# Kernel tuning notes

Measured on AMD Instinct MI355X. Metric: run time of the kernel, lower is better.

The kernel has to match this reference:

```python
import jax, jax.numpy as jnp
import numpy as np

N_NODES_PER_SLICE = 1024  # n_physical_qubits + 1


def _gcn_layer(x, row, col, n_nodes, W, b):
    """PyG GCNConv: add self-loops, symmetric deg normalization, linear, scatter-add, +bias."""
    sl = jnp.arange(n_nodes, dtype=row.dtype)
    row_f = jnp.concatenate([row, sl])
    col_f = jnp.concatenate([col, sl])
    deg = jax.ops.segment_sum(jnp.ones_like(col_f, dtype=x.dtype), col_f, num_segments=n_nodes)
    dinv = jnp.where(deg > 0, jax.lax.rsqrt(deg), 0.0)
    norm = dinv[row_f] * dinv[col_f]            # [E_total]
    h = x @ W                                    # [n_nodes, out]
    msg = h[row_f] * norm[:, None]               # gather + scale
    out = jax.ops.segment_sum(msg, col_f, num_segments=n_nodes)  # scatter-add
    return out + b


def reference(edge_index, qubit_embeddings, W1, b1, W2, b2, W3, b3):
    B = edge_index.shape[0]
    npn = N_NODES_PER_SLICE
    n_nodes = B * npn
    # Batch.from_data_list: offset each slice's edge_index by b * npn, tile node features
    offsets = (jnp.arange(B, dtype=edge_index.dtype) * npn)[:, None]  # [B,1]
    row = (edge_index[:, 0, :] + offsets).reshape(-1)  # [B*E]
    col = (edge_index[:, 1, :] + offsets).reshape(-1)
    x = jnp.tile(qubit_embeddings, (B, 1))             # [B*npn, d0]
    for W, b in ((W1, b1), (W2, b2), (W3, b3)):
        x = jax.nn.relu(_gcn_layer(x, row, col, n_nodes, W, b))
    return x


def setup_inputs() -> dict:
    key = jax.random.key(0)
    ks = jax.random.split(key, 8)
    B, E, d = 512, 2048, 128
    return {
        "edge_index": jax.random.randint(ks[0], (B, 2, E), 0, N_NODES_PER_SLICE, dtype=jnp.int64 if jax.config.jax_enable_x64 else jnp.int32),
        "qubit_embeddings": jax.random.normal(ks[1], (N_NODES_PER_SLICE, d), dtype=jnp.float32),
        "W1": jax.random.normal(ks[2], (d, d), dtype=jnp.float32) * (1.0 / np.sqrt(d)),
        "b1": jnp.zeros((d,), dtype=jnp.float32),
        "W2": jax.random.normal(ks[3], (d, d), dtype=jnp.float32) * (1.0 / np.sqrt(d)),
        "b2": jnp.zeros((d,), dtype=jnp.float32),
        "W3": jax.random.normal(ks[4], (d, d), dtype=jnp.float32) * (1.0 / np.sqrt(d)),
        "b3": jnp.zeros((d,), dtype=jnp.float32),
    }
```

## Files before the change

kernel.cpp:

```cpp
#include <hip/hip_runtime.h>

#define NPN   1024
#define NB    512
#define NE_S  2048
#define DD    128
#define NN    (NB * NPN)
#define NE    (NB * NE_S)

typedef short s16x8 __attribute__((ext_vector_type(8)));
typedef float f32x4 __attribute__((ext_vector_type(4)));

static __device__ __forceinline__ unsigned short f2bf(float f) {
    unsigned u = __builtin_bit_cast(unsigned, f);
    unsigned r = (u + 0x7FFFu + ((u >> 16) & 1u)) >> 16;
    return (unsigned short)r;
}
static __device__ __forceinline__ float bf2f(unsigned short h) {
    unsigned u = ((unsigned)h) << 16;
    return __builtin_bit_cast(float, u);
}


__global__ void k_count(const int* __restrict__ ei, int* __restrict__ deg) {
    int t = blockIdx.x * 256 + threadIdx.x;
    int b = t >> 11, e = t & (NE_S - 1);
    int col = ei[b * (2 * NE_S) + NE_S + e];
    atomicAdd(&deg[b * NPN + col], 1);
}

__global__ void k_dinv(const int* __restrict__ deg, float* __restrict__ dinv) {
    int i = blockIdx.x * 256 + threadIdx.x;
    dinv[i] = rsqrtf((float)(deg[i] + 1));
}

__global__ __launch_bounds__(1024) void k_scan(const int* __restrict__ deg,
                                               int* __restrict__ coff,
                                               int* __restrict__ cur) {
    __shared__ int s[NPN];
    int b = blockIdx.x, t = threadIdx.x;
    int v = deg[b * NPN + t];
    s[t] = v;
    __syncthreads();
    for (int off = 1; off < NPN; off <<= 1) {
        int add = (t >= off) ? s[t - off] : 0;
        __syncthreads();
        s[t] += add;
        __syncthreads();
    }
    coff[b * NPN + t] = b * NE_S + (s[t] - v);
    cur[b * NPN + t] = 0;
}

__global__ void k_fill(const int* __restrict__ ei, const float* __restrict__ dinv,
                       const int* __restrict__ coff, int* __restrict__ cur,
                       int2* __restrict__ cmeta) {
    int t = blockIdx.x * 256 + threadIdx.x;
    int b = t >> 11, e = t & (NE_S - 1);
    int r = ei[b * (2 * NE_S) + e];
    int c = ei[b * (2 * NE_S) + NE_S + e];
    int gr = b * NPN + r, gc = b * NPN + c;
    int pos = coff[gc] + atomicAdd(&cur[gc], 1);
    float nw = dinv[gr] * dinv[gc];
    cmeta[pos] = make_int2(r | (c << 16), __builtin_bit_cast(int, nw));
}


__global__ __launch_bounds__(256) void k_wsplit(const float* __restrict__ W,
                                                short* __restrict__ WTh,
                                                short* __restrict__ WTl) {
    int idx = blockIdx.x * 256 + threadIdx.x;
    int k = idx >> 7, n = idx & 127;
    float f = W[idx];
    unsigned short h = f2bf(f);
    unsigned short l = f2bf(f - bf2f(h));
    WTh[n * DD + k] = (short)h;
    WTl[n * DD + k] = (short)l;
}


__global__ __launch_bounds__(512, 8) void k_layer(const float* __restrict__ x,
                                                  unsigned gmask,
                                                  const short* __restrict__ WTh,
                                                  const short* __restrict__ WTl,
                                                  const float* __restrict__ bias,
                                                  const float* __restrict__ dinv,
                                                  const int* __restrict__ coff,
                                                  const int2* __restrict__ cmeta,
                                                  float* __restrict__ out) {
    __shared__ float sBuf[64 * DD];
    float* sAcc = sBuf;
    char*  sH   = (char*)sBuf;
    char*  sL   = (char*)sBuf + 16384;

    int t = threadIdx.x;
    int wave = t >> 6, lane = t & 63;
    int wb = (int)((blockIdx.x & 7) * 1024 + (blockIdx.x >> 3));
    int m0 = wb * 64;
    int sbase = (wb >> 4) << 10;

    int n  = lane & 15;
    int kq = lane >> 4;

    int r0g = m0 + wave * 8;
    int wlo = (m0 - sbase) + wave * 8;
    int eBeg = __builtin_amdgcn_readfirstlane(coff[r0g]);
    int eEnd = __builtin_amdgcn_readfirstlane((r0g + 8 < NN) ? coff[r0g + 8] : NE);

    int c0 = eBeg;
    int nC0 = eEnd - c0; nC0 = nC0 > 64 ? 64 : nC0;
    int2 md = make_int2((int)0xFFFF0000u, 0);
    if (lane < nC0) md = cmeta[c0 + lane];

    {
        float2 sv[8]; float dvv[8];
        #pragma unroll
        for (int i = 0; i < 8; ++i) {
            int g = m0 + wave * 8 + i;
            dvv[i] = dinv[g];
            sv[i] = *(const float2*)&x[(size_t)((unsigned)g & gmask) * DD + lane * 2];
        }
        #pragma unroll
        for (int i = 0; i < 8; ++i) {
            int row = wave * 8 + i;
            float s = dvv[i] * dvv[i];
            sAcc[row * DD + lane]      = s * sv[i].x;
            sAcc[row * DD + 64 + lane] = s * sv[i].y;
        }
    }

    float ax = 0.f, ay = 0.f;
    int curRow = -1;
    int nC = nC0;
    while (true) {
        int nB = (nC + 15) & ~15;
        for (int b0 = 0; b0 < nB; b0 += 16) {
            float2 v[16];
            #pragma unroll
            for (int j = 0; j < 16; ++j) {
                int sj = __builtin_amdgcn_readlane(md.x, b0 + j) & 0xFFFF;
                v[j] = *(const float2*)&x[(size_t)((unsigned)(sbase + sj) & gmask) * DD + lane * 2];
            }
            #pragma unroll
            for (int j = 0; j < 16; ++j) {
                int pj = __builtin_amdgcn_readlane(md.x, b0 + j);
                int dst = (int)(((unsigned)pj) >> 16);
                float w = __builtin_bit_cast(float, __builtin_amdgcn_readlane(md.y, b0 + j));
                if (dst != curRow) {
                    unsigned rl = (unsigned)(curRow - wlo);
                    if (rl < 8u) {
                        int row = wave * 8 + (int)rl;
                        atomicAdd(&sAcc[row * DD + lane],      ax);
                        atomicAdd(&sAcc[row * DD + 64 + lane], ay);
                    }
                    curRow = dst; ax = 0.f; ay = 0.f;
                }
                ax = fmaf(w, v[j].x, ax);
                ay = fmaf(w, v[j].y, ay);
            }
        }
        c0 += 64;
        if (c0 >= eEnd) break;
        nC = eEnd - c0; nC = nC > 64 ? 64 : nC;
        md = make_int2((int)0xFFFF0000u, 0);
        if (lane < nC) md = cmeta[c0 + lane];
    }
    {
        unsigned rl = (unsigned)(curRow - wlo);
        if (rl < 8u) {
            int row = wave * 8 + (int)rl;
            atomicAdd(&sAcc[row * DD + lane],      ax);
            atomicAdd(&sAcc[row * DD + 64 + lane], ay);
        }
    }
    __syncthreads();

    float fe[8], fo[8];
    #pragma unroll
    for (int i = 0; i < 8; ++i) {
        int row = wave * 8 + i;
        fe[i] = sAcc[row * DD + lane];
        fo[i] = sAcc[row * DD + 64 + lane];
    }
    __syncthreads();
    #pragma unroll
    for (int i = 0; i < 8; ++i) {
        int row = wave * 8 + i;
        unsigned short hx = f2bf(fe[i]); unsigned short lx = f2bf(fe[i] - bf2f(hx));
        unsigned short hy = f2bf(fo[i]); unsigned short ly = f2bf(fo[i] - bf2f(hy));
        unsigned bo = ((unsigned)row * 256u + (unsigned)lane * 4u) ^ ((unsigned)(row & 7) << 4);
        *(unsigned*)(sH + bo) = ((unsigned)hy << 16) | hx;
        *(unsigned*)(sL + bo) = ((unsigned)ly << 16) | lx;
    }
    __syncthreads();

    f32x4 acc[4];
    #pragma unroll
    for (int m = 0; m < 4; ++m) acc[m] = (f32x4){0.f, 0.f, 0.f, 0.f};

    const short* bhp = &WTh[(wave * 16 + n) * DD + kq * 8];
    const short* blp = &WTl[(wave * 16 + n) * DD + kq * 8];
    #pragma unroll
    for (int ks = 0; ks < 4; ++ks) {
        s16x8 bhv = *(const s16x8*)(bhp + ks * 32);
        s16x8 blv = *(const s16x8*)(blp + ks * 32);
        #pragma unroll
        for (int m = 0; m < 4; ++m) {
            int row = m * 16 + n;
            unsigned bo = ((unsigned)row * 256u + (unsigned)(ks * 64 + kq * 16))
                          ^ ((unsigned)(row & 7) << 4);
            s16x8 ah = *(const s16x8*)(sH + bo);
            s16x8 al = *(const s16x8*)(sL + bo);
            acc[m] = __builtin_amdgcn_mfma_f32_16x16x32_bf16(ah, bhv, acc[m], 0, 0, 0);
            acc[m] = __builtin_amdgcn_mfma_f32_16x16x32_bf16(ah, blv, acc[m], 0, 0, 0);
            acc[m] = __builtin_amdgcn_mfma_f32_16x16x32_bf16(al, bhv, acc[m], 0, 0, 0);
        }
    }

    int col = wave * 16 + n;
    float bv = bias[col];
    #pragma unroll
    for (int m = 0; m < 4; ++m) {
        #pragma unroll
        for (int r = 0; r < 4; ++r) {
            int row = m * 16 + kq * 4 + r;
            float vv = acc[m][r] + bv;
            out[(size_t)(m0 + row) * DD + col] = fmaxf(vv, 0.f);
        }
    }
}


extern "C" void kernel_launch(void* const* d_in, const int* in_sizes, int n_in,
                              void* d_out, int out_size, void* d_ws, size_t ws_size,
                              hipStream_t stream) {
    const int*   ei  = (const int*)d_in[0];
    const float* emb = (const float*)d_in[1];
    const float* W1  = (const float*)d_in[2];
    const float* b1  = (const float*)d_in[3];
    const float* W2  = (const float*)d_in[4];
    const float* b2  = (const float*)d_in[5];
    const float* W3  = (const float*)d_in[6];
    const float* b3  = (const float*)d_in[7];
    float* out = (float*)d_out;

    float* x_mid = (float*)d_ws;
    float* dinv  = x_mid + (size_t)NN * DD;
    int*   deg   = (int*)(dinv + NN);
    int*   coff  = deg + NN;
    int*   cur   = coff + NN;
    int2*  cmeta = (int2*)(cur + NN);
    short* WTh1  = (short*)(cmeta + NE);
    short* WTl1  = WTh1 + DD * DD;
    short* WTh2  = WTl1 + DD * DD;
    short* WTl2  = WTh2 + DD * DD;
    short* WTh3  = WTl2 + DD * DD;
    short* WTl3  = WTh3 + DD * DD;

    hipMemsetAsync(deg, 0, NN * sizeof(int), stream);
    k_count<<<NE / 256, 256, 0, stream>>>(ei, deg);
    k_dinv<<<NN / 256, 256, 0, stream>>>(deg, dinv);
    k_scan<<<NB, NPN, 0, stream>>>(deg, coff, cur);
    k_fill<<<NE / 256, 256, 0, stream>>>(ei, dinv, coff, cur, cmeta);

    k_wsplit<<<64, 256, 0, stream>>>(W1, WTh1, WTl1);
    k_wsplit<<<64, 256, 0, stream>>>(W2, WTh2, WTl2);
    k_wsplit<<<64, 256, 0, stream>>>(W3, WTh3, WTl3);

    k_layer<<<NN / 64, 512, 0, stream>>>(emb, NPN - 1, WTh1, WTl1, b1,
                                         dinv, coff, cmeta, out);
    k_layer<<<NN / 64, 512, 0, stream>>>(out, 0xFFFFFFFFu, WTh2, WTl2, b2,
                                         dinv, coff, cmeta, x_mid);
    k_layer<<<NN / 64, 512, 0, stream>>>(x_mid, 0xFFFFFFFFu, WTh3, WTl3, b3,
                                         dinv, coff, cmeta, out);
}
```

Before: 1.123 ms.

## Split wave halves across two edges with float4 gathers and per-edge LDS atomics

Each wave now handles two edges per step, one per 32-lane half, and each lane gathers a float4 from the source row instead of a float2. The per-lane running accumulator keyed on destination row is dropped, and every edge's weighted message goes straight into LDS with four atomic adds. The aim is wider, more coalesced global gathers and half as many serial gather iterations. The cost is many more LDS atomics, since every edge now issues them rather than only at destination changes, and the two halves can contend on the same row. The self-loop initialisation and the later readback are also switched to vector loads and stores.

```diff
diff --git a/kernel.cpp b/kernel.cpp
--- a/kernel.cpp
+++ b/kernel.cpp
@@ -94,6 +94,7 @@
 
     int t = threadIdx.x;
     int wave = t >> 6, lane = t & 63;
+    int half = lane >> 5, li = lane & 31;
     int wb = (int)((blockIdx.x & 7) * 1024 + (blockIdx.x >> 3));
     int m0 = wb * 64;
     int sbase = (wb >> 4) << 10;
@@ -111,51 +112,44 @@
     int2 md = make_int2((int)0xFFFF0000u, 0);
     if (lane < nC0) md = cmeta[c0 + lane];
 
-    {
-        float2 sv[8]; float dvv[8];
-        #pragma unroll
-        for (int i = 0; i < 8; ++i) {
-            int g = m0 + wave * 8 + i;
-            dvv[i] = dinv[g];
-            sv[i] = *(const float2*)&x[(size_t)((unsigned)g & gmask) * DD + lane * 2];
-        }
-        #pragma unroll
-        for (int i = 0; i < 8; ++i) {
-            int row = wave * 8 + i;
-            float s = dvv[i] * dvv[i];
-            sAcc[row * DD + lane]      = s * sv[i].x;
-            sAcc[row * DD + 64 + lane] = s * sv[i].y;
-        }
-    }
-
-    float ax = 0.f, ay = 0.f;
-    int curRow = -1;
+    #pragma unroll
+    for (int i = 0; i < 4; ++i) {
+        int row = wave * 8 + 2 * i + half;
+        int g = m0 + row;
+        float dv = dinv[g];
+        f32x4 v = *(const f32x4*)&x[(size_t)((unsigned)g & gmask) * DD + li * 4];
+        f32x4 sv;
+        sv[0] = dv * dv * v[0]; sv[1] = dv * dv * v[1];
+        sv[2] = dv * dv * v[2]; sv[3] = dv * dv * v[3];
+        *(f32x4*)&sAcc[row * DD + li * 4] = sv;
+    }
+
     int nC = nC0;
     while (true) {
         int nB = (nC + 15) & ~15;
         for (int b0 = 0; b0 < nB; b0 += 16) {
-            float2 v[16];
+            f32x4 v[8]; int mdx[8]; float wv[8];
             #pragma unroll
-            for (int j = 0; j < 16; ++j) {
-                int sj = __builtin_amdgcn_readlane(md.x, b0 + j) & 0xFFFF;
-                v[j] = *(const float2*)&x[(size_t)((unsigned)(sbase + sj) & gmask) * DD + lane * 2];
+            for (int p = 0; p < 8; ++p) {
+                int sA = __builtin_amdgcn_readlane(md.x, b0 + 2 * p);
+                int sB = __builtin_amdgcn_readlane(md.x, b0 + 2 * p + 1);
+                int wA = __builtin_amdgcn_readlane(md.y, b0 + 2 * p);
+                int wB = __builtin_amdgcn_readlane(md.y, b0 + 2 * p + 1);
+                mdx[p] = half ? sB : sA;
+                wv[p]  = __builtin_bit_cast(float, half ? wB : wA);
+                int src = sbase + (mdx[p] & 0xFFFF);
+                v[p] = *(const f32x4*)&x[(size_t)((unsigned)src & gmask) * DD + li * 4];
             }
             #pragma unroll
-            for (int j = 0; j < 16; ++j) {
-                int pj = __builtin_amdgcn_readlane(md.x, b0 + j);
-                int dst = (int)(((unsigned)pj) >> 16);
-                float w = __builtin_bit_cast(float, __builtin_amdgcn_readlane(md.y, b0 + j));
-                if (dst != curRow) {
-                    unsigned rl = (unsigned)(curRow - wlo);
-                    if (rl < 8u) {
-                        int row = wave * 8 + (int)rl;
-                        atomicAdd(&sAcc[row * DD + lane],      ax);
-                        atomicAdd(&sAcc[row * DD + 64 + lane], ay);
-                    }
-                    curRow = dst; ax = 0.f; ay = 0.f;
+            for (int p = 0; p < 8; ++p) {
+                unsigned rl = (((unsigned)mdx[p]) >> 16) - (unsigned)wlo;
+                if (rl < 8u) {
+                    float* ap = &sAcc[(wave * 8 + (int)rl) * DD + li * 4];
+                    atomicAdd(&ap[0], wv[p] * v[p][0]);
+                    atomicAdd(&ap[1], wv[p] * v[p][1]);
+                    atomicAdd(&ap[2], wv[p] * v[p][2]);
+                    atomicAdd(&ap[3], wv[p] * v[p][3]);
                 }
-                ax = fmaf(w, v[j].x, ax);
-                ay = fmaf(w, v[j].y, ay);
             }
         }
         c0 += 64;
@@ -164,22 +158,14 @@
         md = make_int2((int)0xFFFF0000u, 0);
         if (lane < nC) md = cmeta[c0 + lane];
     }
-    {
-        unsigned rl = (unsigned)(curRow - wlo);
-        if (rl < 8u) {
-            int row = wave * 8 + (int)rl;
-            atomicAdd(&sAcc[row * DD + lane],      ax);
-            atomicAdd(&sAcc[row * DD + 64 + lane], ay);
-        }
-    }
     __syncthreads();
 
     float fe[8], fo[8];
     #pragma unroll
     for (int i = 0; i < 8; ++i) {
         int row = wave * 8 + i;
-        fe[i] = sAcc[row * DD + lane];
-        fo[i] = sAcc[row * DD + 64 + lane];
+        float2 p2 = *(const float2*)&sAcc[row * DD + lane * 2];
+        fe[i] = p2.x; fo[i] = p2.y;
     }
     __syncthreads();
     #pragma unroll
```

Result: slower. 2.285 ms (+103.5%).
